# Performance work log

Measured on AMD Instinct MI355X. Metric: run time of the kernel, lower is better.

Reference implementation:

```python
import jax, jax.numpy as jnp
import numpy as np

COMPLEXES = 2048
RESX = 16
RESY = 16
RATE = 16
FEAT = 64


def setup_inputs() -> dict:
    key = jax.random.key(0)
    k1, k2, k3 = jax.random.split(key, 3)
    P = RATE * RATE  # samples per complex
    map_ = jax.random.normal(k1, (COMPLEXES, RESY, RESX, FEAT), dtype=jnp.float32)
    u = jax.random.uniform(k2, (COMPLEXES, P), dtype=jnp.float32)
    v = jax.random.uniform(k3, (COMPLEXES, P), dtype=jnp.float32)
    return {"map": map_, "u": u, "v": v}


def reference(map, u, v):
    # map: [complexes, resy, resx, feat]; u, v: [complexes, P] in [0,1]
    C, H, W, F = map.shape
    x = u * (W - 1)
    y = v * (H - 1)
    x0 = jnp.clip(jnp.floor(x).astype(jnp.int32), 0, W - 2)
    y0 = jnp.clip(jnp.floor(y).astype(jnp.int32), 0, H - 2)
    fx = (x - x0.astype(x.dtype))[..., None]  # [C, P, 1]
    fy = (y - y0.astype(y.dtype))[..., None]
    cidx = jnp.arange(C)[:, None]  # [C, 1] broadcast over samples
    g00 = map[cidx, y0, x0]          # [C, P, F]
    g01 = map[cidx, y0, x0 + 1]
    g10 = map[cidx, y0 + 1, x0]
    g11 = map[cidx, y0 + 1, x0 + 1]
    top = g00 * (1.0 - fx) + g01 * fx
    bot = g10 * (1.0 - fx) + g11 * fx
    return top * (1.0 - fy) + bot * fy  # [C, P, F]
```

## Files before the change

### kernel.cpp

```cpp
#include <hip/hip_runtime.h>

constexpr int C_ = 2048;
constexpr int H_ = 16;
constexpr int W_ = 16;
constexpr int F_ = 64;
constexpr int P_ = 256;

__global__ __launch_bounds__(256) void ngf_fetch_kernel(
    const float* __restrict__ map_,
    const float* __restrict__ u_,
    const float* __restrict__ v_,
    float* __restrict__ out_) {
  __shared__ float4 s_w[P_];
  __shared__ int    s_ix[P_];

  const int c = blockIdx.x;
  const int tid = threadIdx.x;

  {
    const float x = u_[(size_t)c * P_ + tid] * (float)(W_ - 1);
    const float y = v_[(size_t)c * P_ + tid] * (float)(H_ - 1);
    int x0 = (int)floorf(x);
    int y0 = (int)floorf(y);
    x0 = x0 < 0 ? 0 : (x0 > W_ - 2 ? W_ - 2 : x0);
    y0 = y0 < 0 ? 0 : (y0 > H_ - 2 ? H_ - 2 : y0);
    const float fx = x - (float)x0;
    const float fy = y - (float)y0;
    const float wx0 = 1.0f - fx;
    const float wy0 = 1.0f - fy;
    s_w[tid] = make_float4(wx0 * wy0, fx * wy0, wx0 * fy, fx * fy);
    s_ix[tid] = (y0 * W_ + x0) * (F_ / 4);
  }
  __syncthreads();

  const float4* __restrict__ gmap =
      (const float4*)(map_ + (size_t)c * (H_ * W_ * F_));
  float4* __restrict__ gout = (float4*)(out_ + (size_t)c * (P_ * F_));
  const int f = tid & 15;
  const int sbase = tid >> 4;

#pragma unroll
  for (int it = 0; it < 16; ++it) {
    const int s = it * 16 + sbase;
    const float4 w = s_w[s];
    const int ix = s_ix[s] + f;

    const float4 g00 = gmap[ix];
    const float4 g01 = gmap[ix + (F_ / 4)];
    const float4 g10 = gmap[ix + W_ * (F_ / 4)];
    const float4 g11 = gmap[ix + (W_ + 1) * (F_ / 4)];

    float4 r;
    r.x = g00.x * w.x + g01.x * w.y + g10.x * w.z + g11.x * w.w;
    r.y = g00.y * w.x + g01.y * w.y + g10.y * w.z + g11.y * w.w;
    r.z = g00.z * w.x + g01.z * w.y + g10.z * w.z + g11.z * w.w;
    r.w = g00.w * w.x + g01.w * w.y + g10.w * w.z + g11.w * w.w;

    gout[s * (F_ / 4) + f] = r;
  }
}

extern "C" void kernel_launch(void* const* d_in, const int* in_sizes, int n_in,
                              void* d_out, int out_size, void* d_ws, size_t ws_size,
                              hipStream_t stream) {
  const float* map_ = (const float*)d_in[0];
  const float* u_   = (const float*)d_in[1];
  const float* v_   = (const float*)d_in[2];
  float* out_ = (float*)d_out;

  ngf_fetch_kernel<<<C_, 256, 0, stream>>>(map_, u_, v_, out_);
}
```

Baseline: 260.0 us.

## Split each complex across 16 blocks with XCD-aware mapping, drop shared memory

Each complex is now handled by 16 blocks instead of one, and each thread processes a single sample-feature pair rather than looping 16 times. Block indices are remapped so that all blocks for a given complex land on the same XCD, which keeps the complex's 64KB map slice in that die's L2. The shared-memory weight precompute and the barrier are removed, and each thread computes its own weights. The trade-off is 16x more blocks, redundant weight and u/v computation per thread, and less in-thread memory-level parallelism.

```diff
diff --git a/kernel.cpp b/kernel.cpp
--- a/kernel.cpp
+++ b/kernel.cpp
@@ -5,59 +5,51 @@
 constexpr int W_ = 16;
 constexpr int F_ = 64;
 constexpr int P_ = 256;
+constexpr int CHUNK = 16;
+constexpr int NB = C_ * (P_ / CHUNK);
 
-__global__ __launch_bounds__(256) void ngf_fetch_kernel(
+
+__global__ __launch_bounds__(256, 8) void ngf_fetch_kernel(
     const float* __restrict__ map_,
     const float* __restrict__ u_,
     const float* __restrict__ v_,
     float* __restrict__ out_) {
-  __shared__ float4 s_w[P_];
-  __shared__ int    s_ix[P_];
+  const int b = blockIdx.x;
+  const int xcd  = b & 7;
+  const int slot = b >> 3;
+  const int c    = (xcd << 8) | (slot >> 4);
+  const int k    = slot & 15;
 
-  const int c = blockIdx.x;
   const int tid = threadIdx.x;
+  const int f = tid & 15;
+  const int s = (k << 4) | (tid >> 4);
 
-  {
-    const float x = u_[(size_t)c * P_ + tid] * (float)(W_ - 1);
-    const float y = v_[(size_t)c * P_ + tid] * (float)(H_ - 1);
-    int x0 = (int)floorf(x);
-    int y0 = (int)floorf(y);
-    x0 = x0 < 0 ? 0 : (x0 > W_ - 2 ? W_ - 2 : x0);
-    y0 = y0 < 0 ? 0 : (y0 > H_ - 2 ? H_ - 2 : y0);
-    const float fx = x - (float)x0;
-    const float fy = y - (float)y0;
-    const float wx0 = 1.0f - fx;
-    const float wy0 = 1.0f - fy;
-    s_w[tid] = make_float4(wx0 * wy0, fx * wy0, wx0 * fy, fx * fy);
-    s_ix[tid] = (y0 * W_ + x0) * (F_ / 4);
-  }
-  __syncthreads();
+  const float x = u_[(size_t)c * P_ + s] * (float)(W_ - 1);
+  const float y = v_[(size_t)c * P_ + s] * (float)(H_ - 1);
+  int x0 = (int)floorf(x);
+  int y0 = (int)floorf(y);
+  x0 = x0 < 0 ? 0 : (x0 > W_ - 2 ? W_ - 2 : x0);
+  y0 = y0 < 0 ? 0 : (y0 > H_ - 2 ? H_ - 2 : y0);
+  const float wx1 = x - (float)x0, wx0 = 1.0f - wx1;
+  const float wy1 = y - (float)y0, wy0 = 1.0f - wy1;
 
   const float4* __restrict__ gmap =
       (const float4*)(map_ + (size_t)c * (H_ * W_ * F_));
+  const int ix = (y0 * W_ + x0) * (F_ / 4) + f;
+
+  const float4 g00 = gmap[ix];
+  const float4 g01 = gmap[ix + (F_ / 4)];
+  const float4 g10 = gmap[ix + W_ * (F_ / 4)];
+  const float4 g11 = gmap[ix + (W_ + 1) * (F_ / 4)];
+
+  float4 r;
+  r.x = (g00.x * wx0 + g01.x * wx1) * wy0 + (g10.x * wx0 + g11.x * wx1) * wy1;
+  r.y = (g00.y * wx0 + g01.y * wx1) * wy0 + (g10.y * wx0 + g11.y * wx1) * wy1;
+  r.z = (g00.z * wx0 + g01.z * wx1) * wy0 + (g10.z * wx0 + g11.z * wx1) * wy1;
+  r.w = (g00.w * wx0 + g01.w * wx1) * wy0 + (g10.w * wx0 + g11.w * wx1) * wy1;
+
   float4* __restrict__ gout = (float4*)(out_ + (size_t)c * (P_ * F_));
-  const int f = tid & 15;
-  const int sbase = tid >> 4;
-
-#pragma unroll
-  for (int it = 0; it < 16; ++it) {
-    const int s = it * 16 + sbase;
-    const float4 w = s_w[s];
-    const int ix = s_ix[s] + f;
-
-    const float4 g00 = gmap[ix];
-    const float4 g01 = gmap[ix + (F_ / 4)];
-    const float4 g10 = gmap[ix + W_ * (F_ / 4)];
-    const float4 g11 = gmap[ix + (W_ + 1) * (F_ / 4)];
-
-    float4 r;
-    r.x = g00.x * w.x + g01.x * w.y + g10.x * w.z + g11.x * w.w;
-    r.y = g00.y * w.x + g01.y * w.y + g10.y * w.z + g11.y * w.w;
-    r.z = g00.z * w.x + g01.z * w.y + g10.z * w.z + g11.z * w.w;
-    r.w = g00.w * w.x + g01.w * w.y + g10.w * w.z + g11.w * w.w;
-
-    gout[s * (F_ / 4) + f] = r;
-  }
+  gout[s * (F_ / 4) + f] = r;
 }
 
 extern "C" void kernel_launch(void* const* d_in, const int* in_sizes, int n_in,
@@ -68,5 +60,5 @@
   const float* v_   = (const float*)d_in[2];
   float* out_ = (float*)d_out;
 
-  ngf_fetch_kernel<<<C_, 256, 0, stream>>>(map_, u_, v_, out_);
+  ngf_fetch_kernel<<<NB, 256, 0, stream>>>(map_, u_, v_, out_);
 }
```

Result: faster. 250.4 us (-3.7%).
